# Performance work log

Hardware: AMD Instinct MI355X
Metric: run time of the kernel (lower is better)

## Reference

```python
import jax, jax.numpy as jnp
import numpy as np

B, H, L, D = 2, 16, 1024, 64
LMAX = 2048  # max_sequence_length: patterns built & normalized at LMAX, then sliced to L
PI = float(np.pi)


def _scale_pattern(freq):
    # pattern[h, t, d] = exp(i(t+ph)) + exp(i(2t+ph)) + exp(i(0.5t+ph)), ph = 2*pi*h/H
    # identical across d, so keep [H, L, 1] and broadcast over D
    phase = 2.0 * PI * jnp.arange(H, dtype=jnp.float32) / H          # [H]
    t = jnp.linspace(0.0, 2.0 * PI * freq, LMAX)                     # [LMAX]
    a1 = t[None, :] + phase[:, None]
    a2 = 2.0 * t[None, :] + phase[:, None]
    a3 = 0.5 * t[None, :] + phase[:, None]
    pr = jnp.cos(a1) + jnp.cos(a2) + jnp.cos(a3)                     # [H, LMAX]
    pi_ = jnp.sin(a1) + jnp.sin(a2) + jnp.sin(a3)
    norm = jnp.sqrt(jnp.sum(pr * pr + pi_ * pi_, axis=1, keepdims=True))  # over full LMAX
    pr, pi_ = pr / norm, pi_ / norm
    return pr[:, :L, None], pi_[:, :L, None]                          # [H, L, 1]


def _expert_total_pattern():
    # 8 experts x 3 aspects; pattern[t, d] = exp(i(f*t + 2*pi*d/D)), normalized per
    # column over LMAX (|exp|=1 -> norm sqrt(LMAX)). Elementwise complex multiply is
    # linear, so the expert stage equals x * sum(all patterns)/(sqrt(3)*sqrt(8)).
    freqs = np.array([[0.3 + 0.1 * i, 0.2 + 0.1 * i, 0.1 + 0.1 * i]
                      for i in range(8)], dtype=np.float32).reshape(-1)   # [24]
    t = jnp.linspace(0.0, 2.0 * PI, LMAX)                                 # [LMAX]
    phase_d = 2.0 * PI * jnp.arange(D, dtype=jnp.float32) / D             # [D]
    ang = jnp.asarray(freqs)[:, None, None] * t[None, :, None] + phase_d[None, None, :]  # [24, LMAX, D]
    col_norm = 1.0 / np.sqrt(float(LMAX))
    denom = np.sqrt(3.0) * np.sqrt(8.0)
    pr = jnp.sum(jnp.cos(ang), axis=0) * (col_norm / denom)               # [LMAX, D]
    pi_ = jnp.sum(jnp.sin(ang), axis=0) * (col_norm / denom)
    return pr[:L], pi_[:L]                                                # [L, D]


def _process_scale(Qr, Qi, Kr, Ki, Vr, Vi, pr, pi_):
    # complex elementwise pattern multiply
    Qpr = Qr * pr - Qi * pi_
    Qpi = Qr * pi_ + Qi * pr
    Kpr = Kr * pr - Ki * pi_
    Kpi = Kr * pi_ + Ki * pr
    # complex scores = Qp @ Kp^T (no conjugation, matching the torch code)
    sr = jnp.einsum('bhld,bhmd->bhlm', Qpr, Kpr) - jnp.einsum('bhld,bhmd->bhlm', Qpi, Kpi)
    si = jnp.einsum('bhld,bhmd->bhlm', Qpr, Kpi) + jnp.einsum('bhld,bhmd->bhlm', Qpi, Kpr)
    mag = jnp.sqrt(sr * sr + si * si) / np.sqrt(float(D))
    w = jax.nn.softmax(mag, axis=-1)
    return (jnp.einsum('bhlm,bhmd->bhld', w, Vr),
            jnp.einsum('bhlm,bhmd->bhld', w, Vi))


def reference(Q_real, Q_imag, K_real, K_imag, V_real, V_imag):
    scale_freqs = [1.0, 0.5, 0.25, 0.1]  # char, word, phrase, sentence
    acc_r = jnp.zeros_like(Q_real)
    acc_i = jnp.zeros_like(Q_real)
    for f in scale_freqs:
        pr, pi_ = _scale_pattern(f)
        o_r, o_i = _process_scale(Q_real, Q_imag, K_real, K_imag, V_real, V_imag, pr, pi_)
        acc_r = acc_r + o_r
        acc_i = acc_i + o_i
    inv = 1.0 / np.sqrt(float(len(scale_freqs)))
    acc_r = acc_r * inv
    acc_i = acc_i * inv
    # expert mixing (linear in x -> single fused complex elementwise multiply)
    epr, epi = _expert_total_pattern()  # [L, D], broadcast over B,H
    out_r = acc_r * epr - acc_i * epi
    out_i = acc_r * epi + acc_i * epr
    return jnp.stack([out_r, out_i], axis=0)  # [2, B, H, L, D] (real, imag)


def setup_inputs() -> dict:
    key = jax.random.key(0)
    ks = jax.random.split(key, 6)
    shape = (B, H, L, D)
    names = ['Q_real', 'Q_imag', 'K_real', 'K_imag', 'V_real', 'V_imag']
    return {n: jax.random.normal(k, shape, dtype=jnp.float32) for n, k in zip(names, ks)}
```

## Files before the change

### kernel.cpp

```cpp
#include <hip/hip_runtime.h>
#include <math.h>

typedef short bf16x8 __attribute__((ext_vector_type(8)));
typedef float f32x4 __attribute__((ext_vector_type(4)));

#define BDIM 256
constexpr int B_ = 2, H_ = 16, L_ = 1024, D_ = 64, LMAX_ = 2048;
constexpr int BH_ = B_ * H_;
constexpr float PI_F = 3.14159265358979323846f;

constexpr int WS_SVP = 0;
constexpr int WS_KBR = 65536;
constexpr int WS_KBI = WS_KBR + 1048576;
constexpr int WS_VTR = WS_KBI + 1048576;
constexpr int WS_VTI = WS_VTR + 1048576;

__device__ __forceinline__ unsigned short f2b(float x) {
    union { float f; unsigned u; } v; v.f = x;
    return (unsigned short)((v.u + 0x8000u) >> 16);
}
__device__ __forceinline__ unsigned pk2(float a, float b) {
    union { float f; unsigned u; } va, vb; va.f = a; vb.f = b;
    return ((va.u + 0x8000u) >> 16) | ((vb.u + 0x8000u) & 0xFFFF0000u);
}
__device__ __forceinline__ uint4 pack4(const float4& a, const float4& b) {
    return make_uint4(pk2(a.x, a.y), pk2(a.z, a.w), pk2(b.x, b.y), pk2(b.z, b.w));
}

#define MFMA(a, b, c) __builtin_amdgcn_mfma_f32_16x16x32_bf16((a), (b), (c), 0, 0, 0)

__device__ __forceinline__ float a_val(int s, int l, float4 invn) {
    const float fr = (s == 0) ? 1.0f : (s == 1) ? 0.5f : (s == 2) ? 0.25f : 0.1f;
    const float iv = (s == 0) ? invn.x : (s == 1) ? invn.y : (s == 2) ? invn.z : invn.w;
    float t = (2.0f * PI_F * fr / (float)(LMAX_ - 1)) * (float)l;
    float m2 = 3.0f + 2.0f * cosf(t) + 2.0f * cosf(0.5f * t) + 2.0f * cosf(1.5f * t);
    return sqrtf(fmaxf(m2, 0.0f)) * iv;
}

__global__ __launch_bounds__(BDIM)
void prep_kernel(const float* __restrict__ Kr, const float* __restrict__ Ki,
                 const float* __restrict__ Vr, const float* __restrict__ Vi,
                 float* __restrict__ ws) {
    const int tid = threadIdx.x;
    const int blk = blockIdx.x;
    unsigned short* KbR = (unsigned short*)(ws + WS_KBR);
    unsigned short* KbI = (unsigned short*)(ws + WS_KBI);
    unsigned short* VtR = (unsigned short*)(ws + WS_VTR);
    unsigned short* VtI = (unsigned short*)(ws + WS_VTI);

    if (blk < 256) {
        const int comp = blk >> 7;
        const float* src = comp ? Ki : Kr;
        unsigned short* dst = comp ? KbI : KbR;
        size_t b0 = (size_t)(blk & 127) * 16384;
#pragma unroll
        for (int i = 0; i < 4; ++i) {
            size_t e = b0 + (size_t)(i * 256 + tid) * 16;
            float4 x0 = *(const float4*)(src + e);
            float4 x1 = *(const float4*)(src + e + 4);
            float4 x2 = *(const float4*)(src + e + 8);
            float4 x3 = *(const float4*)(src + e + 12);
            *(uint4*)(dst + e) = pack4(x0, x1);
            *(uint4*)(dst + e + 8) = pack4(x2, x3);
        }
    } else {
        __shared__ unsigned short sT[64 * 68];
        __shared__ float sRed[4 * 64];
        const int vb = blk - 256;
        const int comp = vb & 1, mt = (vb >> 1) & 15, bh = vb >> 5;
        const int m0 = mt * 64;
        const float* src = (comp ? Vi : Vr) + (size_t)bh * 65536 + (size_t)m0 * 64;
        unsigned short* dstA = (comp ? VtI : VtR) + (size_t)bh * 65536;
#pragma unroll
        for (int i = 0; i < 4; ++i) {
            int e = i * 256 + tid;
            int m = e >> 4, d4 = (e & 15) * 4;
            float4 x = *(const float4*)(src + (size_t)m * 64 + d4);
            *(uint2*)&sT[m * 68 + d4] = make_uint2(pk2(x.x, x.y), pk2(x.z, x.w));
        }
        {
            int d = tid & 63, grp = tid >> 6;
            float s = 0.0f;
#pragma unroll
            for (int k = 0; k < 16; ++k) s += src[(size_t)(grp * 16 + k) * 64 + d];
            sRed[grp * 64 + d] = s;
        }
        __syncthreads();
        {
            int d = tid >> 2, ms = (tid & 3) * 16;
            unsigned short v[16];
#pragma unroll
            for (int k = 0; k < 16; ++k) v[k] = sT[(ms + k) * 68 + d];
            unsigned short* dst = dstA + (size_t)d * 1024 + m0 + ms;
            *(uint4*)dst = make_uint4((unsigned)v[0] | ((unsigned)v[1] << 16),
                                      (unsigned)v[2] | ((unsigned)v[3] << 16),
                                      (unsigned)v[4] | ((unsigned)v[5] << 16),
                                      (unsigned)v[6] | ((unsigned)v[7] << 16));
            *(uint4*)(dst + 8) = make_uint4((unsigned)v[8] | ((unsigned)v[9] << 16),
                                            (unsigned)v[10] | ((unsigned)v[11] << 16),
                                            (unsigned)v[12] | ((unsigned)v[13] << 16),
                                            (unsigned)v[14] | ((unsigned)v[15] << 16));
        }
        if (tid < 64)
            ws[WS_SVP + comp * 32768 + bh * 1024 + mt * 64 + tid] =
                sRed[tid] + sRed[64 + tid] + sRed[128 + tid] + sRed[192 + tid];
    }
}

__device__ __forceinline__ void stage64s(const unsigned short* g0, int stride,
                                         unsigned short* lds, int w, int lane) {
#pragma unroll
    for (int i = 0; i < 2; ++i) {
        int c = w * 2 + i;
        int lrow = c * 8 + (lane >> 3);
        int lg = (lane & 7) ^ (lrow & 7);
        const unsigned short* src = g0 + (size_t)lrow * stride + lg * 8;
        __builtin_amdgcn_global_load_lds(
            (const __attribute__((address_space(1))) void*)src,
            (__attribute__((address_space(3))) void*)(lds + c * 512), 16, 0, 0);
    }
}
__device__ __forceinline__ bf16x8 ldfrag(const unsigned short* b, int row, int g) {
    return *(const bf16x8*)&b[row * 64 + ((g ^ (row & 7)) << 3)];
}
__device__ __forceinline__ bf16x8 ldfragE(const unsigned short* b, int row, int g) {
    return *(const bf16x8*)&b[row * 72 + ((g ^ (row & 7)) << 3)];
}

__global__ __launch_bounds__(BDIM, 2)
void attn_kernel(const float* __restrict__ Qr, const float* __restrict__ Qi,
                 const float* __restrict__ ws, float* __restrict__ out, float4 invn) {
    __shared__ unsigned short sK0[4096], sK1[4096];
    __shared__ unsigned short sV0[4096], sV1[4096];
    __shared__ unsigned short sE[64 * 72];
    __shared__ unsigned short sMg[64 * 72];
    __shared__ unsigned short sAmb[4 * 1032];
    __shared__ float sDen[4 * 64];

    const int tid = threadIdx.x;
    const int lane = tid & 63;
    const int w = tid >> 6;
    const int lo16 = lane & 15;
    const int quad = lane >> 4;
    const int blk = blockIdx.x;
    const int bh = (blk & 7) * 4 + (blk >> 7);
    const int qt = (blk >> 3) & 15;
    const int l0 = qt * 64;
    const size_t base = (size_t)bh * (L_ * D_);

    const unsigned short* gKr = (const unsigned short*)(ws + WS_KBR) + (size_t)bh * 65536;
    const unsigned short* gKi = (const unsigned short*)(ws + WS_KBI) + (size_t)bh * 65536;
    const unsigned short* gVr = (const unsigned short*)(ws + WS_VTR) + (size_t)bh * 65536;
    const unsigned short* gVi = (const unsigned short*)(ws + WS_VTI) + (size_t)bh * 65536;

    for (int e = tid; e < 4096; e += BDIM) {
        int s = e >> 10, l = e & 1023;
        sAmb[s * 1032 + l] = f2b(a_val(s, l, invn) * 0.125f);
    }

    bf16x8 fQr0, fQr1, fQi0, fQi1, fnQi0, fnQi1;
    {
        const int ql = l0 + w * 16 + lo16;
        const float* qr = Qr + base + (size_t)ql * 64;
        const float* qi = Qi + base + (size_t)ql * 64;
        float4 a0 = *(const float4*)(qr + quad * 8);
        float4 a1 = *(const float4*)(qr + quad * 8 + 4);
        float4 b0 = *(const float4*)(qr + 32 + quad * 8);
        float4 b1 = *(const float4*)(qr + 32 + quad * 8 + 4);
        *(uint4*)&fQr0 = pack4(a0, a1);
        *(uint4*)&fQr1 = pack4(b0, b1);
        a0 = *(const float4*)(qi + quad * 8);
        a1 = *(const float4*)(qi + quad * 8 + 4);
        b0 = *(const float4*)(qi + 32 + quad * 8);
        b1 = *(const float4*)(qi + 32 + quad * 8 + 4);
        *(uint4*)&fQi0 = pack4(a0, a1);
        *(uint4*)&fQi1 = pack4(b0, b1);
        uint4 t0 = *(uint4*)&fQi0, t1 = *(uint4*)&fQi1;
        t0.x ^= 0x80008000u; t0.y ^= 0x80008000u; t0.z ^= 0x80008000u; t0.w ^= 0x80008000u;
        t1.x ^= 0x80008000u; t1.y ^= 0x80008000u; t1.z ^= 0x80008000u; t1.w ^= 0x80008000u;
        *(uint4*)&fnQi0 = t0; *(uint4*)&fnQi1 = t1;
    }

    bf16x8 uf1a = (bf16x8){0, 0, 0, 0, 0, 0, 0, 0};
    uf1a[0] = (short)f2b(a_val(quad, l0 + w * 16 + lo16, invn) * (1.0f / 1024.0f));

    f32x4 accM1 = (f32x4){0.f, 0.f, 0.f, 0.f};
    f32x4 aOutR[4], aOutI[4];
#pragma unroll
    for (int dt = 0; dt < 4; ++dt) {
        aOutR[dt] = (f32x4){0.f, 0.f, 0.f, 0.f};
        aOutI[dt] = (f32x4){0.f, 0.f, 0.f, 0.f};
    }

#pragma unroll 1
    for (int mt = 0; mt < 16; ++mt) {
        const int m0 = mt * 64;
        __syncthreads();
        stage64s(gKr + (size_t)m0 * 64, 64, sK0, w, lane);
        stage64s(gKi + (size_t)m0 * 64, 64, sK1, w, lane);
        stage64s(gVr + m0, 1024, sV0, w, lane);
        stage64s(gVi + m0, 1024, sV1, w, lane);
        __syncthreads();

#pragma unroll
        for (int ct = 0; ct < 4; ++ct) {
            const int mrow = ct * 16 + lo16;
            bf16x8 kr0 = ldfrag(sK0, mrow, quad), kr1 = ldfrag(sK0, mrow, quad + 4);
            bf16x8 ki0 = ldfrag(sK1, mrow, quad), ki1 = ldfrag(sK1, mrow, quad + 4);
            f32x4 aR = (f32x4){0.f, 0.f, 0.f, 0.f};
            f32x4 aI = (f32x4){0.f, 0.f, 0.f, 0.f};
            aR = MFMA(kr0, fQr0, aR);  aR = MFMA(kr1, fQr1, aR);
            aR = MFMA(ki0, fnQi0, aR); aR = MFMA(ki1, fnQi1, aR);
            aI = MFMA(ki0, fQr0, aI);  aI = MFMA(ki1, fQr1, aI);
            aI = MFMA(kr0, fQi0, aI);  aI = MFMA(kr1, fQi1, aI);
            float mg0 = sqrtf(fmaf(aR[0], aR[0], aI[0] * aI[0]));
            float mg1 = sqrtf(fmaf(aR[1], aR[1], aI[1] * aI[1]));
            float mg2 = sqrtf(fmaf(aR[2], aR[2], aI[2] * aI[2]));
            float mg3 = sqrtf(fmaf(aR[3], aR[3], aI[3] * aI[3]));
            bf16x8 bf1 = (bf16x8){0, 0, 0, 0, 0, 0, 0, 0};
            bf1[0] = (short)sAmb[quad * 1032 + m0 + ct * 16 + lo16];
            f32x4 z = (f32x4){0.f, 0.f, 0.f, 0.f};
            f32x4 a1 = MFMA(bf1, uf1a, z);
            float p0 = mg0 * a1[0], p1 = mg1 * a1[1];
            float p2 = mg2 * a1[2], p3 = mg3 * a1[3];
            int l = w * 16 + lo16;
            int gph = (ct * 2 + (quad >> 1)) ^ (l & 7);
            *(uint2*)&sE[l * 72 + gph * 8 + (quad & 1) * 4] =
                make_uint2(pk2(p0, p1), pk2(p2, p3));
            *(uint2*)&sMg[l * 72 + gph * 8 + (quad & 1) * 4] =
                make_uint2(pk2(mg0, mg1), pk2(mg2, mg3));
        }
        {
            bf16x8 mf0 = ldfragE(sMg, w * 16 + lo16, quad);
            bf16x8 mf1 = ldfragE(sMg, w * 16 + lo16, quad + 4);
            bf16x8 b0 = (bf16x8){0, 0, 0, 0, 0, 0, 0, 0};
            bf16x8 b1 = (bf16x8){0, 0, 0, 0, 0, 0, 0, 0};
            if (lo16 < 4) {
                b0 = *(const bf16x8*)&sAmb[lo16 * 1032 + m0 + quad * 8];
                b1 = *(const bf16x8*)&sAmb[lo16 * 1032 + m0 + 32 + quad * 8];
            }
            accM1 = MFMA(mf0, b0, accM1);
            accM1 = MFMA(mf1, b1, accM1);
        }
        {
            bf16x8 pa0 = ldfragE(sE, w * 16 + lo16, quad);
            bf16x8 pa1 = ldfragE(sE, w * 16 + lo16, quad + 4);
#pragma unroll
            for (int dt = 0; dt < 4; ++dt) {
                int dr = dt * 16 + lo16;
                bf16x8 vr0 = ldfrag(sV0, dr, quad), vr1 = ldfrag(sV0, dr, quad + 4);
                bf16x8 vi0 = ldfrag(sV1, dr, quad), vi1 = ldfrag(sV1, dr, quad + 4);
                aOutR[dt] = MFMA(pa0, vr0, aOutR[dt]);
                aOutR[dt] = MFMA(pa1, vr1, aOutR[dt]);
                aOutI[dt] = MFMA(pa0, vi0, aOutI[dt]);
                aOutI[dt] = MFMA(pa1, vi1, aOutI[dt]);
            }
        }
    }

    if (lo16 < 4) {
#pragma unroll
        for (int reg = 0; reg < 4; ++reg) {
            int r = w * 16 + quad * 4 + reg;
            float alv = a_val(lo16, l0 + r, invn);
            sDen[lo16 * 64 + r] = 1.0f / (1024.0f + alv * accM1[reg]);
        }
    }
    float cden[4];
#pragma unroll
    for (int reg = 0; reg < 4; ++reg) {
        int r = w * 16 + quad * 4 + reg;
        cden[reg] = sDen[r] + sDen[64 + r] + sDen[128 + r] + sDen[192 + r];
    }

    const float cE = rsqrtf(2048.0f) * rsqrtf(24.0f);
    float eRr[4], eRi[4];
#pragma unroll
    for (int reg = 0; reg < 4; ++reg) {
        int lrow = l0 + w * 16 + quad * 4 + reg;
        float tl = (2.0f * PI_F / (float)(LMAX_ - 1)) * (float)lrow;
        float s1, c1;
        __sincosf(0.1f * tl, &s1, &c1);
        const float W[10] = {1.f, 2.f, 3.f, 3.f, 3.f, 3.f, 3.f, 3.f, 2.f, 1.f};
        float cr = c1, ci = s1;
        float er = W[0] * cr, ei = W[0] * ci;
#pragma unroll
        for (int k = 1; k < 10; ++k) {
            float nr = cr * c1 - ci * s1;
            float ni = cr * s1 + ci * c1;
            cr = nr; ci = ni;
            er = fmaf(W[k], cr, er);
            ei = fmaf(W[k], ci, ei);
        }
        eRr[reg] = er * cE;
        eRi[reg] = ei * cE;
    }

    const size_t ooff = (size_t)BH_ * L_ * D_;
#pragma unroll
    for (int dt = 0; dt < 4; ++dt) {
        int d = dt * 16 + lo16;
        float svr = 0.0f, svi = 0.0f;
#pragma unroll
        for (int q = 0; q < 16; ++q) {
            svr += ws[WS_SVP + bh * 1024 + q * 64 + d];
            svi += ws[WS_SVP + 32768 + bh * 1024 + q * 64 + d];
        }
        float sp, cp;
        __sincosf((2.0f * PI_F / 64.0f) * (float)d, &sp, &cp);
#pragma unroll
        for (int reg = 0; reg < 4; ++reg) {
            int lrow = l0 + w * 16 + quad * 4 + reg;
            float numR = fmaf(cden[reg], svr, aOutR[dt][reg]) * 0.5f;
            float numI = fmaf(cden[reg], svi, aOutI[dt][reg]) * 0.5f;
            float epr = cp * eRr[reg] - sp * eRi[reg];
            float epi = sp * eRr[reg] + cp * eRi[reg];
            size_t o = base + (size_t)lrow * 64 + d;
            out[o] = numR * epr - numI * epi;
            out[o + ooff] = numR * epi + numI * epr;
        }
    }
}

extern "C" void kernel_launch(void* const* d_in, const int* in_sizes, int n_in,
                              void* d_out, int out_size, void* d_ws, size_t ws_size,
                              hipStream_t stream) {
    const float* Qr = (const float*)d_in[0];
    const float* Qi = (const float*)d_in[1];
    const float* Kr = (const float*)d_in[2];
    const float* Ki = (const float*)d_in[3];
    const float* Vr = (const float*)d_in[4];
    const float* Vi = (const float*)d_in[5];
    float* ws = (float*)d_ws;
    float* out = (float*)d_out;

    const double fr[4] = {1.0, 0.5, 0.25, 0.1};
    float inv[4];
    for (int s = 0; s < 4; ++s) {
        double a = 2.0 * 3.14159265358979323846 * fr[s] / (double)(LMAX_ - 1);
        double S = 3.0 * LMAX_;
        const double mul[3] = {1.0, 0.5, 1.5};
        for (int k = 0; k < 3; ++k) {
            double x = a * mul[k];
            S += 2.0 * (cos(x * 1023.5) * sin(x * 1024.0) / sin(x * 0.5));
        }
        inv[s] = (float)(1.0 / sqrt(S));
    }
    float4 invn = make_float4(inv[0], inv[1], inv[2], inv[3]);

    prep_kernel<<<1280, BDIM, 0, stream>>>(Kr, Ki, Vr, Vi, ws);
    attn_kernel<<<512, BDIM, 0, stream>>>(Qr, Qi, ws, out, invn);
}
```

Before: 158.4 us.

## Double-buffer K tiles, overlap V loads with score compute, add MFMA priority

K real/imag tiles become double-buffered: the next tile is prefetched while the current one is used, and V tiles are issued at loop start so their loads overlap the score MFMAs. Explicit vmcnt waits and raw barriers replace the two __syncthreads per iteration. The sE/sMg padding is dropped in favour of the XOR-swizzled 64-wide layout, the transpose scratch stride changes from 68 to 70, and s_setprio is raised around the MFMA blocks. This costs more LDS per block and relies on hand-counted vmcnt values, which may limit occupancy or break if the compiler reorders memory ops.

```diff
diff --git a/kernel.cpp b/kernel.cpp
--- a/kernel.cpp
+++ b/kernel.cpp
@@ -64,7 +64,7 @@
             *(uint4*)(dst + e + 8) = pack4(x2, x3);
         }
     } else {
-        __shared__ unsigned short sT[64 * 68];
+        __shared__ unsigned short sT[64 * 70];
         __shared__ float sRed[4 * 64];
         const int vb = blk - 256;
         const int comp = vb & 1, mt = (vb >> 1) & 15, bh = vb >> 5;
@@ -76,7 +76,7 @@
             int e = i * 256 + tid;
             int m = e >> 4, d4 = (e & 15) * 4;
             float4 x = *(const float4*)(src + (size_t)m * 64 + d4);
-            *(uint2*)&sT[m * 68 + d4] = make_uint2(pk2(x.x, x.y), pk2(x.z, x.w));
+            *(uint2*)&sT[m * 70 + d4] = make_uint2(pk2(x.x, x.y), pk2(x.z, x.w));
         }
         {
             int d = tid & 63, grp = tid >> 6;
@@ -90,7 +90,7 @@
             int d = tid >> 2, ms = (tid & 3) * 16;
             unsigned short v[16];
 #pragma unroll
-            for (int k = 0; k < 16; ++k) v[k] = sT[(ms + k) * 68 + d];
+            for (int k = 0; k < 16; ++k) v[k] = sT[(ms + k) * 70 + d];
             unsigned short* dst = dstA + (size_t)d * 1024 + m0 + ms;
             *(uint4*)dst = make_uint4((unsigned)v[0] | ((unsigned)v[1] << 16),
                                       (unsigned)v[2] | ((unsigned)v[3] << 16),
@@ -123,17 +123,14 @@
 __device__ __forceinline__ bf16x8 ldfrag(const unsigned short* b, int row, int g) {
     return *(const bf16x8*)&b[row * 64 + ((g ^ (row & 7)) << 3)];
 }
-__device__ __forceinline__ bf16x8 ldfragE(const unsigned short* b, int row, int g) {
-    return *(const bf16x8*)&b[row * 72 + ((g ^ (row & 7)) << 3)];
-}
 
 __global__ __launch_bounds__(BDIM, 2)
 void attn_kernel(const float* __restrict__ Qr, const float* __restrict__ Qi,
                  const float* __restrict__ ws, float* __restrict__ out, float4 invn) {
-    __shared__ unsigned short sK0[4096], sK1[4096];
+    __shared__ unsigned short sK0[2][4096], sK1[2][4096];
     __shared__ unsigned short sV0[4096], sV1[4096];
-    __shared__ unsigned short sE[64 * 72];
-    __shared__ unsigned short sMg[64 * 72];
+    __shared__ unsigned short sE[4096];
+    __shared__ unsigned short sMg[4096];
     __shared__ unsigned short sAmb[4 * 1032];
     __shared__ float sDen[4 * 64];
 
@@ -152,6 +149,9 @@
     const unsigned short* gKi = (const unsigned short*)(ws + WS_KBI) + (size_t)bh * 65536;
     const unsigned short* gVr = (const unsigned short*)(ws + WS_VTR) + (size_t)bh * 65536;
     const unsigned short* gVi = (const unsigned short*)(ws + WS_VTI) + (size_t)bh * 65536;
+
+    stage64s(gKr, 64, sK0[0], w, lane);
+    stage64s(gKi, 64, sK1[0], w, lane);
 
     for (int e = tid; e < 4096; e += BDIM) {
         int s = e >> 10, l = e & 1023;
@@ -192,27 +192,34 @@
         aOutI[dt] = (f32x4){0.f, 0.f, 0.f, 0.f};
     }
 
+    __syncthreads();
+
+    int cur = 0;
 #pragma unroll 1
     for (int mt = 0; mt < 16; ++mt) {
         const int m0 = mt * 64;
-        __syncthreads();
-        stage64s(gKr + (size_t)m0 * 64, 64, sK0, w, lane);
-        stage64s(gKi + (size_t)m0 * 64, 64, sK1, w, lane);
         stage64s(gVr + m0, 1024, sV0, w, lane);
         stage64s(gVi + m0, 1024, sV1, w, lane);
-        __syncthreads();
+        if (mt < 15) {
+            stage64s(gKr + (size_t)(m0 + 64) * 64, 64, sK0[cur ^ 1], w, lane);
+            stage64s(gKi + (size_t)(m0 + 64) * 64, 64, sK1[cur ^ 1], w, lane);
+        }
+        const unsigned short* cK0 = sK0[cur];
+        const unsigned short* cK1 = sK1[cur];
 
 #pragma unroll
         for (int ct = 0; ct < 4; ++ct) {
             const int mrow = ct * 16 + lo16;
-            bf16x8 kr0 = ldfrag(sK0, mrow, quad), kr1 = ldfrag(sK0, mrow, quad + 4);
-            bf16x8 ki0 = ldfrag(sK1, mrow, quad), ki1 = ldfrag(sK1, mrow, quad + 4);
+            bf16x8 kr0 = ldfrag(cK0, mrow, quad), kr1 = ldfrag(cK0, mrow, quad + 4);
+            bf16x8 ki0 = ldfrag(cK1, mrow, quad), ki1 = ldfrag(cK1, mrow, quad + 4);
             f32x4 aR = (f32x4){0.f, 0.f, 0.f, 0.f};
             f32x4 aI = (f32x4){0.f, 0.f, 0.f, 0.f};
+            __builtin_amdgcn_s_setprio(1);
             aR = MFMA(kr0, fQr0, aR);  aR = MFMA(kr1, fQr1, aR);
             aR = MFMA(ki0, fnQi0, aR); aR = MFMA(ki1, fnQi1, aR);
             aI = MFMA(ki0, fQr0, aI);  aI = MFMA(ki1, fQr1, aI);
             aI = MFMA(kr0, fQi0, aI);  aI = MFMA(kr1, fQi1, aI);
+            __builtin_amdgcn_s_setprio(0);
             float mg0 = sqrtf(fmaf(aR[0], aR[0], aI[0] * aI[0]));
             float mg1 = sqrtf(fmaf(aR[1], aR[1], aI[1] * aI[1]));
             float mg2 = sqrtf(fmaf(aR[2], aR[2], aI[2] * aI[2]));
@@ -225,14 +232,14 @@
             float p2 = mg2 * a1[2], p3 = mg3 * a1[3];
             int l = w * 16 + lo16;
             int gph = (ct * 2 + (quad >> 1)) ^ (l & 7);
-            *(uint2*)&sE[l * 72 + gph * 8 + (quad & 1) * 4] =
+            *(uint2*)&sE[l * 64 + gph * 8 + (quad & 1) * 4] =
                 make_uint2(pk2(p0, p1), pk2(p2, p3));
-            *(uint2*)&sMg[l * 72 + gph * 8 + (quad & 1) * 4] =
+            *(uint2*)&sMg[l * 64 + gph * 8 + (quad & 1) * 4] =
                 make_uint2(pk2(mg0, mg1), pk2(mg2, mg3));
         }
         {
-            bf16x8 mf0 = ldfragE(sMg, w * 16 + lo16, quad);
-            bf16x8 mf1 = ldfragE(sMg, w * 16 + lo16, quad + 4);
+            bf16x8 mf0 = ldfrag(sMg, w * 16 + lo16, quad);
+            bf16x8 mf1 = ldfrag(sMg, w * 16 + lo16, quad + 4);
             bf16x8 b0 = (bf16x8){0, 0, 0, 0, 0, 0, 0, 0};
             bf16x8 b1 = (bf16x8){0, 0, 0, 0, 0, 0, 0, 0};
             if (lo16 < 4) {
@@ -242,9 +249,16 @@
             accM1 = MFMA(mf0, b0, accM1);
             accM1 = MFMA(mf1, b1, accM1);
         }
+        if (mt < 15) {
+            asm volatile("s_waitcnt vmcnt(4)" ::: "memory");
+        } else {
+            asm volatile("s_waitcnt vmcnt(0)" ::: "memory");
+        }
+        __builtin_amdgcn_s_barrier();
         {
-            bf16x8 pa0 = ldfragE(sE, w * 16 + lo16, quad);
-            bf16x8 pa1 = ldfragE(sE, w * 16 + lo16, quad + 4);
+            bf16x8 pa0 = ldfrag(sE, w * 16 + lo16, quad);
+            bf16x8 pa1 = ldfrag(sE, w * 16 + lo16, quad + 4);
+            __builtin_amdgcn_s_setprio(1);
 #pragma unroll
             for (int dt = 0; dt < 4; ++dt) {
                 int dr = dt * 16 + lo16;
@@ -255,7 +269,11 @@
                 aOutI[dt] = MFMA(pa0, vi0, aOutI[dt]);
                 aOutI[dt] = MFMA(pa1, vi1, aOutI[dt]);
             }
-        }
+            __builtin_amdgcn_s_setprio(0);
+        }
+        asm volatile("s_waitcnt vmcnt(0)" ::: "memory");
+        __builtin_amdgcn_s_barrier();
+        cur ^= 1;
     }
 
     if (lo16 < 4) {
```

Result: faster. 152.2 us (-3.9%).
